# Kernel optimization log

Measured on AMD Instinct MI355X. Metric: run time of the kernel, lower is better.

## Reference

```python
import jax, jax.numpy as jnp
import numpy as np

M_MARGIN = 0.25
GAMMA = 256.0
NEG_INF = jnp.float32(-1e30)


def setup_inputs() -> dict:
    key = jax.random.key(0)
    k1, k2 = jax.random.split(key)
    feature = jax.random.normal(k1, (8192, 128), dtype=jnp.float32)
    label = jax.random.randint(k2, (8192,), 0, 64, dtype=jnp.int64)
    return {"feature": feature, "label": label}


def reference(feature, label):
    # F.normalize: L2-normalize rows (eps=1e-12)
    norm = jnp.maximum(jnp.linalg.norm(feature, axis=1, keepdims=True), 1e-12)
    f = feature / norm
    sim = f @ f.T  # [N, N]
    N = sim.shape[0]

    same = label[:, None] == label[None, :]
    triu = jnp.triu(jnp.ones((N, N), dtype=bool), k=1)
    pos_mask = same & triu
    neg_mask = (~same) & triu

    sim_d = jax.lax.stop_gradient(sim)  # .detach() in original
    ap = jnp.maximum(-sim_d + 1.0 + M_MARGIN, 0.0)
    an = jnp.maximum(sim_d + M_MARGIN, 0.0)
    delta_p = 1.0 - M_MARGIN
    delta_n = M_MARGIN

    logit_p = -ap * (sim - delta_p) * GAMMA
    logit_n = an * (sim - delta_n) * GAMMA

    # boolean-gather + logsumexp == masked logsumexp (fixed shapes, jit-friendly)
    lse_p = jax.nn.logsumexp(jnp.where(pos_mask, logit_p, NEG_INF))
    lse_n = jax.nn.logsumexp(jnp.where(neg_mask, logit_n, NEG_INF))

    return jax.nn.softplus(lse_n + lse_p)
```

## Files before the change

kernel.cpp:

```cpp
#include <hip/hip_runtime.h>
#include <hip/hip_bf16.h>
#include <math.h>

#define NROW 8192
#define DIM  128
#define BT   128
#define NT   (NROW / BT)
#define NBLK ((NT * (NT + 1)) / 2)
#define NWR  (NBLK * 4)

typedef __bf16 bf16x8 __attribute__((ext_vector_type(8)));
typedef float  f32x4  __attribute__((ext_vector_type(4)));

#define G2     369.3299304675746f
#define QPOS   (0.9375f * G2)
#define QNEG   (-0.0625f * G2)
#define NEGBIG (-3.0e38f)
#define MSENT  (-4000.0f)

__global__ __launch_bounds__(256)
void prep_kernel(const float* __restrict__ f, __hip_bfloat16* __restrict__ fhi) {
    int row  = blockIdx.x * 4 + (threadIdx.x >> 6);
    int lane = threadIdx.x & 63;
    float2 v = ((const float2*)(f + (size_t)row * DIM))[lane];
    float ss = v.x * v.x + v.y * v.y;
    #pragma unroll
    for (int off = 32; off; off >>= 1) ss += __shfl_xor(ss, off, 64);
    float inv = 1.0f / fmaxf(sqrtf(ss), 1e-12f);
    __hip_bfloat162 hv;
    hv.x = __float2bfloat16(v.x * inv);
    hv.y = __float2bfloat16(v.y * inv);
    ((__hip_bfloat162*)(fhi + (size_t)row * DIM))[lane] = hv;
}

__global__ __launch_bounds__(256, 2)
void sim_kernel(const __hip_bfloat16* __restrict__ fhi,
                const int* __restrict__ lab,
                float4* __restrict__ blockRes) {
    const int tid  = threadIdx.x;
    const int w    = tid >> 6;
    const int lane = tid & 63;
    const int lrow = lane & 15;
    const int lk   = lane >> 4;

    int bid = blockIdx.x;
    int tr = (int)((129.0f - sqrtf(16641.0f - 8.0f * (float)bid)) * 0.5f);
    while (tr > 0 && bid < tr * NT - (tr * (tr - 1)) / 2) --tr;
    while (bid >= (tr + 1) * NT - ((tr + 1) * tr) / 2) ++tr;
    const int tc = tr + (bid - (tr * NT - (tr * (tr - 1)) / 2));

    const int rowBase = tr * BT;
    const int colBase = tc * BT;
    const bool edge = (tr == tc);

    __shared__ __align__(16) char smem[64 * 1024];
    __shared__ int labA[BT];
    __shared__ int labB[BT];
    char* As = smem;
    char* Bs = smem + 32 * 1024;

    if (tid < BT)            labA[tid] = lab[rowBase + tid];
    else if (tid < 2 * BT)   labB[tid - BT] = lab[colBase + (tid - BT)];

    const int rsub4 = lane >> 4;
    const int col16 = (lane & 15) << 4;

    #pragma unroll
    for (int t = 0; t < 16; ++t) {
        int seg = w * 16 + t;
        int arr = seg >> 5;
        int s32 = seg & 31;
        int row = s32 * 4 + rsub4;
        const char* g = (const char*)fhi
            + (size_t)((arr ? colBase : rowBase) + row) * 256
            + (col16 ^ ((row & 7) << 4));
        char* ldsb = (arr ? Bs : As) + s32 * 1024;
        __builtin_amdgcn_global_load_lds(
            (const __attribute__((address_space(1))) void*)g,
            (__attribute__((address_space(3))) void*)ldsb, 16, 0, 0);
    }

    f32x4 acc[4][4];
    #pragma unroll
    for (int mi = 0; mi < 4; ++mi)
        #pragma unroll
        for (int ni = 0; ni < 4; ++ni) acc[mi][ni] = (f32x4){0.f, 0.f, 0.f, 0.f};

    const int mrow0 = (w >> 1) * 64;
    const int ncol0 = (w & 1) * 64;

    __syncthreads();

    #pragma unroll
    for (int q = 0; q < 4; ++q) {
        const int kb = q * 64 + lk * 16;
        bf16x8 bfr[4];
        #pragma unroll
        for (int ni = 0; ni < 4; ++ni) {
            int rb = colBase ? (ncol0 + ni * 16 + lrow) : (ncol0 + ni * 16 + lrow);
            rb = ncol0 + ni * 16 + lrow;
            bfr[ni] = *(const bf16x8*)(Bs + rb * 256 + (kb ^ ((rb & 7) << 4)));
        }
        bf16x8 afr[4];
        #pragma unroll
        for (int mi = 0; mi < 4; ++mi) {
            int ra = mrow0 + mi * 16 + lrow;
            afr[mi] = *(const bf16x8*)(As + ra * 256 + (kb ^ ((ra & 7) << 4)));
        }
        #pragma unroll
        for (int mi = 0; mi < 4; ++mi)
            #pragma unroll
            for (int ni = 0; ni < 4; ++ni)
                acc[mi][ni] = __builtin_amdgcn_mfma_f32_16x16x32_bf16(
                    afr[mi], bfr[ni], acc[mi][ni], 0, 0, 0);
    }

    int lbv[4];
    #pragma unroll
    for (int ni = 0; ni < 4; ++ni) lbv[ni] = labB[ncol0 + ni * 16 + lrow];
    int4 laR[4];
    #pragma unroll
    for (int mi = 0; mi < 4; ++mi)
        laR[mi] = *(const int4*)&labA[mrow0 + mi * 16 + lk * 4];

    float minp = 1e30f;
    float mabs = -1.0f;

#define PASS_A(EDGEF)                                                          \
    _Pragma("unroll")                                                          \
    for (int mi = 0; mi < 4; ++mi) {                                           \
        const int la[4] = {laR[mi].x, laR[mi].y, laR[mi].z, laR[mi].w};        \
        _Pragma("unroll")                                                      \
        for (int ni = 0; ni < 4; ++ni) {                                       \
            _Pragma("unroll")                                                  \
            for (int r = 0; r < 4; ++r) {                                      \
                float s = acc[mi][ni][r];                                      \
                bool pos = (la[r] == lbv[ni]);                                 \
                float t = fmaxf(s, -0.25f);                                    \
                bool valid = true;                                             \
                if (EDGEF) {                                                   \
                    int il = mrow0 + mi * 16 + lk * 4 + r;                     \
                    int jl = ncol0 + ni * 16 + lrow;                           \
                    valid = (jl > il);                                         \
                    pos = pos && valid;                                        \
                }                                                              \
                float u = pos ? s : t;                                         \
                minp = fminf(minp, pos ? s : 1e30f);                           \
                bool nm = EDGEF ? (valid && !pos) : !pos;                      \
                mabs = fmaxf(mabs, nm ? fabsf(t) : -1.0f);                     \
                acc[mi][ni][r] = u;                                            \
            }                                                                  \
        }                                                                      \
    }
    if (edge) { PASS_A(true) } else { PASS_A(false) }
#undef PASS_A

    #pragma unroll
    for (int off = 32; off; off >>= 1) {
        minp = fminf(minp, __shfl_xor(minp, off, 64));
        mabs = fmaxf(mabs, __shfl_xor(mabs, off, 64));
    }
    const float Mp = (minp < 2.0f)
        ? fmaf(G2, minp * minp, fmaf(-2.0f * G2, minp, QPOS)) : MSENT;
    const float Mn = (mabs >= 0.0f) ? fmaf(G2, mabs * mabs, QNEG) : MSENT;
    const float qph = QPOS - Mp;
    const float qnh = QNEG - Mn;
    float sp = 0.f, sn = 0.f;

#define PASS_B(EDGEF)                                                          \
    _Pragma("unroll")                                                          \
    for (int mi = 0; mi < 4; ++mi) {                                           \
        const int la[4] = {laR[mi].x, laR[mi].y, laR[mi].z, laR[mi].w};        \
        _Pragma("unroll")                                                      \
        for (int ni = 0; ni < 4; ++ni) {                                       \
            _Pragma("unroll")                                                  \
            for (int r = 0; r < 4; ++r) {                                      \
                float u = acc[mi][ni][r];                                      \
                bool pos = (la[r] == lbv[ni]);                                 \
                float P  = pos ? (-2.0f * G2) : 0.0f;                          \
                float Qh = pos ? qph : qnh;                                    \
                float e = __builtin_amdgcn_exp2f(                              \
                              fmaf(G2, u * u, fmaf(P, u, Qh)));                \
                if (EDGEF) {                                                   \
                    int il = mrow0 + mi * 16 + lk * 4 + r;                     \
                    int jl = ncol0 + ni * 16 + lrow;                           \
                    e = (jl > il) ? e : 0.f;                                   \
                }                                                              \
                float ep = pos ? e : 0.f;                                      \
                sp += ep;                                                      \
                sn += (e - ep);                                                \
            }                                                                  \
        }                                                                      \
    }
    if (edge) { PASS_B(true) } else { PASS_B(false) }
#undef PASS_B

    #pragma unroll
    for (int off = 32; off; off >>= 1) {
        sp += __shfl_xor(sp, off, 64);
        sn += __shfl_xor(sn, off, 64);
    }
    if (lane == 0) blockRes[bid * 4 + w] = make_float4(Mp, sp, Mn, sn);
}

__global__ __launch_bounds__(1024)
void final_kernel(const float4* __restrict__ waveRes, float* __restrict__ out) {
    __shared__ float red[16][4];
    const int tid  = threadIdx.x;
    const int wv   = tid >> 6;
    const int lane = tid & 63;

    float4 e[9];
    int ne = 0;
    for (int i = tid; i < NWR; i += 1024) e[ne++] = waveRes[i];

    float mp = NEGBIG, mn = NEGBIG;
    for (int k = 0; k < ne; ++k) {
        mp = fmaxf(mp, e[k].x);
        mn = fmaxf(mn, e[k].z);
    }
    #pragma unroll
    for (int off = 32; off; off >>= 1) {
        mp = fmaxf(mp, __shfl_xor(mp, off, 64));
        mn = fmaxf(mn, __shfl_xor(mn, off, 64));
    }
    if (lane == 0) { red[wv][0] = mp; red[wv][1] = mn; }
    __syncthreads();
    float MP = red[0][0], MN = red[0][1];
    #pragma unroll
    for (int q = 1; q < 16; ++q) {
        MP = fmaxf(MP, red[q][0]);
        MN = fmaxf(MN, red[q][1]);
    }

    float sp = 0.f, sn = 0.f;
    for (int k = 0; k < ne; ++k) {
        sp = fmaf(e[k].y, __builtin_amdgcn_exp2f(e[k].x - MP), sp);
        sn = fmaf(e[k].w, __builtin_amdgcn_exp2f(e[k].z - MN), sn);
    }
    #pragma unroll
    for (int off = 32; off; off >>= 1) {
        sp += __shfl_xor(sp, off, 64);
        sn += __shfl_xor(sn, off, 64);
    }
    __syncthreads();
    if (lane == 0) { red[wv][2] = sp; red[wv][3] = sn; }
    __syncthreads();
    if (tid == 0) {
        float Sp = 0.f, Sn = 0.f;
        #pragma unroll
        for (int q = 0; q < 16; ++q) { Sp += red[q][2]; Sn += red[q][3]; }
        const double LN2 = 0.6931471805599453;
        double lse_p = ((double)MP + log2((double)Sp)) * LN2;
        double lse_n = ((double)MN + log2((double)Sn)) * LN2;
        double xx = lse_p + lse_n;
        double r = (xx > 30.0) ? xx : log1p(exp(xx));
        out[0] = (float)r;
    }
}

extern "C" void kernel_launch(void* const* d_in, const int* in_sizes, int n_in,
                              void* d_out, int out_size, void* d_ws, size_t ws_size,
                              hipStream_t stream) {
    const float* f   = (const float*)d_in[0];
    const int*   lab = (const int*)d_in[1];
    float*  out      = (float*)d_out;

    __hip_bfloat16* fhi = (__hip_bfloat16*)d_ws;
    float4* blockRes = (float4*)((char*)d_ws + 4u * 1024 * 1024);

    prep_kernel<<<NROW / 4, 256, 0, stream>>>(f, fhi);
    sim_kernel<<<NBLK, 256, 0, stream>>>(fhi, lab, blockRes);
    final_kernel<<<1, 1024, 0, stream>>>(blockRes, out);
}
```

Baseline: 55.73 us.

## Sort rows by label so pure-negative tiles skip label masking

Adds a label histogram and prefix-sum kernel, then scatters the normalized rows into label-sorted order with an atomic cursor. Tiles whose row and column label ranges cannot overlap take a cheaper path with no positive branch and no per-element label comparisons. The sim kernel also moves to 512 threads with 8 waves on smaller 64x32 sub-tiles, and merges per-wave logsumexp partials into one result per block, which shrinks the final reduction. The cost is an extra launch plus atomics in prep, and the atomic scatter makes row order nondeterministic, which can change float summation order.

After: 51.67 us. -7.3%, faster.

```diff
diff --git a/kernel.cpp b/kernel.cpp
--- a/kernel.cpp
+++ b/kernel.cpp
@@ -7,7 +7,6 @@
 #define BT   128
 #define NT   (NROW / BT)
 #define NBLK ((NT * (NT + 1)) / 2)
-#define NWR  (NBLK * 4)
 
 typedef __bf16 bf16x8 __attribute__((ext_vector_type(8)));
 typedef float  f32x4  __attribute__((ext_vector_type(4)));
@@ -17,9 +16,35 @@
 #define QNEG   (-0.0625f * G2)
 #define NEGBIG (-3.0e38f)
 #define MSENT  (-4000.0f)
+#define CSTR   32
 
 __global__ __launch_bounds__(256)
-void prep_kernel(const float* __restrict__ f, __hip_bfloat16* __restrict__ fhi) {
+void hist_kernel(const int* __restrict__ lab, int* __restrict__ cursor) {
+    __shared__ int h[4][64];
+    const int tid  = threadIdx.x;
+    const int w    = tid >> 6;
+    const int lane = tid & 63;
+    h[w][lane] = 0;
+    __syncthreads();
+    for (int i = tid; i < NROW; i += 256)
+        atomicAdd(&h[w][lab[i]], 1);
+    __syncthreads();
+    if (tid < 64) {
+        int tot = h[0][tid] + h[1][tid] + h[2][tid] + h[3][tid];
+        int v = tot;
+        #pragma unroll
+        for (int off = 1; off < 64; off <<= 1) {
+            int u = __shfl_up(v, off, 64);
+            if (tid >= off) v += u;
+        }
+        cursor[tid * CSTR] = v - tot;
+    }
+}
+
+__global__ __launch_bounds__(256)
+void prep_kernel(const float* __restrict__ f, const int* __restrict__ lab,
+                 int* __restrict__ cursor,
+                 __hip_bfloat16* __restrict__ fhi, int* __restrict__ labS) {
     int row  = blockIdx.x * 4 + (threadIdx.x >> 6);
     int lane = threadIdx.x & 63;
     float2 v = ((const float2*)(f + (size_t)row * DIM))[lane];
@@ -27,15 +52,26 @@
     #pragma unroll
     for (int off = 32; off; off >>= 1) ss += __shfl_xor(ss, off, 64);
     float inv = 1.0f / fmaxf(sqrtf(ss), 1e-12f);
+    int l = lab[row];
+    int dest = 0;
+    if (lane == 0) dest = atomicAdd(&cursor[l * CSTR], 1);
+    dest = __shfl(dest, 0, 64);
     __hip_bfloat162 hv;
     hv.x = __float2bfloat16(v.x * inv);
     hv.y = __float2bfloat16(v.y * inv);
-    ((__hip_bfloat162*)(fhi + (size_t)row * DIM))[lane] = hv;
-}
-
-__global__ __launch_bounds__(256, 2)
+    ((__hip_bfloat162*)(fhi + (size_t)dest * DIM))[lane] = hv;
+    if (lane == 0) labS[dest] = l;
+}
+
+__device__ __forceinline__ void merge2(float& m, float& s, float mo, float so) {
+    float M = fmaxf(m, mo);
+    s = s * __builtin_amdgcn_exp2f(m - M) + so * __builtin_amdgcn_exp2f(mo - M);
+    m = M;
+}
+
+__global__ __launch_bounds__(512, 4)
 void sim_kernel(const __hip_bfloat16* __restrict__ fhi,
-                const int* __restrict__ lab,
+                const int* __restrict__ labS,
                 float4* __restrict__ blockRes) {
     const int tid  = threadIdx.x;
     const int w    = tid >> 6;
@@ -54,20 +90,16 @@
     const bool edge = (tr == tc);
 
     __shared__ __align__(16) char smem[64 * 1024];
-    __shared__ int labA[BT];
-    __shared__ int labB[BT];
+    __shared__ float red[8][4];
     char* As = smem;
     char* Bs = smem + 32 * 1024;
 
-    if (tid < BT)            labA[tid] = lab[rowBase + tid];
-    else if (tid < 2 * BT)   labB[tid - BT] = lab[colBase + (tid - BT)];
-
     const int rsub4 = lane >> 4;
     const int col16 = (lane & 15) << 4;
 
     #pragma unroll
-    for (int t = 0; t < 16; ++t) {
-        int seg = w * 16 + t;
+    for (int t = 0; t < 8; ++t) {
+        int seg = w * 8 + t;
         int arr = seg >> 5;
         int s32 = seg & 31;
         int row = s32 * 4 + rsub4;
@@ -80,58 +112,91 @@
             (__attribute__((address_space(3))) void*)ldsb, 16, 0, 0);
     }
 
-    f32x4 acc[4][4];
+    const bool pure = (!edge) && (labS[rowBase + BT - 1] != labS[colBase]);
+
+    const int mrow0 = (w >> 2) * 64;
+    const int ncol0 = (w & 3) * 32;
+
+    int lbv[2];
+    int4 laR[4];
+    if (!pure) {
+        #pragma unroll
+        for (int ni = 0; ni < 2; ++ni) lbv[ni] = labS[colBase + ncol0 + ni * 16 + lrow];
+        #pragma unroll
+        for (int mi = 0; mi < 4; ++mi)
+            laR[mi] = *(const int4*)&labS[rowBase + mrow0 + mi * 16 + lk * 4];
+    }
+
+    f32x4 acc[4][2];
     #pragma unroll
     for (int mi = 0; mi < 4; ++mi)
         #pragma unroll
-        for (int ni = 0; ni < 4; ++ni) acc[mi][ni] = (f32x4){0.f, 0.f, 0.f, 0.f};
-
-    const int mrow0 = (w >> 1) * 64;
-    const int ncol0 = (w & 1) * 64;
+        for (int ni = 0; ni < 2; ++ni) acc[mi][ni] = (f32x4){0.f, 0.f, 0.f, 0.f};
 
     __syncthreads();
 
     #pragma unroll
     for (int q = 0; q < 4; ++q) {
         const int kb = q * 64 + lk * 16;
-        bf16x8 bfr[4];
-        #pragma unroll
-        for (int ni = 0; ni < 4; ++ni) {
-            int rb = colBase ? (ncol0 + ni * 16 + lrow) : (ncol0 + ni * 16 + lrow);
-            rb = ncol0 + ni * 16 + lrow;
+        bf16x8 bfr[2];
+        #pragma unroll
+        for (int ni = 0; ni < 2; ++ni) {
+            int rb = ncol0 + ni * 16 + lrow;
             bfr[ni] = *(const bf16x8*)(Bs + rb * 256 + (kb ^ ((rb & 7) << 4)));
         }
-        bf16x8 afr[4];
         #pragma unroll
         for (int mi = 0; mi < 4; ++mi) {
             int ra = mrow0 + mi * 16 + lrow;
-            afr[mi] = *(const bf16x8*)(As + ra * 256 + (kb ^ ((ra & 7) << 4)));
-        }
+            bf16x8 afr = *(const bf16x8*)(As + ra * 256 + (kb ^ ((ra & 7) << 4)));
+            #pragma unroll
+            for (int ni = 0; ni < 2; ++ni)
+                acc[mi][ni] = __builtin_amdgcn_mfma_f32_16x16x32_bf16(
+                    afr, bfr[ni], acc[mi][ni], 0, 0, 0);
+        }
+    }
+
+    float Mp, Mn, sp, sn;
+    if (pure) {
+        float mx = 0.0f;
         #pragma unroll
         for (int mi = 0; mi < 4; ++mi)
             #pragma unroll
-            for (int ni = 0; ni < 4; ++ni)
-                acc[mi][ni] = __builtin_amdgcn_mfma_f32_16x16x32_bf16(
-                    afr[mi], bfr[ni], acc[mi][ni], 0, 0, 0);
-    }
-
-    int lbv[4];
-    #pragma unroll
-    for (int ni = 0; ni < 4; ++ni) lbv[ni] = labB[ncol0 + ni * 16 + lrow];
-    int4 laR[4];
-    #pragma unroll
-    for (int mi = 0; mi < 4; ++mi)
-        laR[mi] = *(const int4*)&labA[mrow0 + mi * 16 + lk * 4];
-
-    float minp = 1e30f;
-    float mabs = -1.0f;
+            for (int ni = 0; ni < 2; ++ni)
+                #pragma unroll
+                for (int r = 0; r < 4; ++r) {
+                    float t = fmaxf(acc[mi][ni][r], -0.25f);
+                    acc[mi][ni][r] = t;
+                    mx = fmaxf(mx, fabsf(t));
+                }
+        #pragma unroll
+        for (int off = 32; off; off >>= 1)
+            mx = fmaxf(mx, __shfl_xor(mx, off, 64));
+        const float zc = -G2 * mx * mx;
+        sn = 0.f;
+        #pragma unroll
+        for (int mi = 0; mi < 4; ++mi)
+            #pragma unroll
+            for (int ni = 0; ni < 2; ++ni)
+                #pragma unroll
+                for (int r = 0; r < 4; ++r) {
+                    float t = acc[mi][ni][r];
+                    sn += __builtin_amdgcn_exp2f(fmaf(G2, t * t, zc));
+                }
+        #pragma unroll
+        for (int off = 32; off; off >>= 1)
+            sn += __shfl_xor(sn, off, 64);
+        Mp = MSENT; sp = 0.f;
+        Mn = fmaf(G2, mx * mx, QNEG);
+    } else {
+        float minp = 1e30f;
+        float mabs = -1.0f;
 
 #define PASS_A(EDGEF)                                                          \
     _Pragma("unroll")                                                          \
     for (int mi = 0; mi < 4; ++mi) {                                           \
         const int la[4] = {laR[mi].x, laR[mi].y, laR[mi].z, laR[mi].w};        \
         _Pragma("unroll")                                                      \
-        for (int ni = 0; ni < 4; ++ni) {                                       \
+        for (int ni = 0; ni < 2; ++ni) {                                       \
             _Pragma("unroll")                                                  \
             for (int r = 0; r < 4; ++r) {                                      \
                 float s = acc[mi][ni][r];                                      \
@@ -152,27 +217,27 @@
             }                                                                  \
         }                                                                      \
     }
-    if (edge) { PASS_A(true) } else { PASS_A(false) }
+        if (edge) { PASS_A(true) } else { PASS_A(false) }
 #undef PASS_A
 
-    #pragma unroll
-    for (int off = 32; off; off >>= 1) {
-        minp = fminf(minp, __shfl_xor(minp, off, 64));
-        mabs = fmaxf(mabs, __shfl_xor(mabs, off, 64));
-    }
-    const float Mp = (minp < 2.0f)
-        ? fmaf(G2, minp * minp, fmaf(-2.0f * G2, minp, QPOS)) : MSENT;
-    const float Mn = (mabs >= 0.0f) ? fmaf(G2, mabs * mabs, QNEG) : MSENT;
-    const float qph = QPOS - Mp;
-    const float qnh = QNEG - Mn;
-    float sp = 0.f, sn = 0.f;
+        #pragma unroll
+        for (int off = 32; off; off >>= 1) {
+            minp = fminf(minp, __shfl_xor(minp, off, 64));
+            mabs = fmaxf(mabs, __shfl_xor(mabs, off, 64));
+        }
+        Mp = (minp < 2.0f)
+            ? fmaf(G2, minp * minp, fmaf(-2.0f * G2, minp, QPOS)) : MSENT;
+        Mn = (mabs >= 0.0f) ? fmaf(G2, mabs * mabs, QNEG) : MSENT;
+        const float qph = QPOS - Mp;
+        const float qnh = QNEG - Mn;
+        sp = 0.f; sn = 0.f;
 
 #define PASS_B(EDGEF)                                                          \
     _Pragma("unroll")                                                          \
     for (int mi = 0; mi < 4; ++mi) {                                           \
         const int la[4] = {laR[mi].x, laR[mi].y, laR[mi].z, laR[mi].w};        \
         _Pragma("unroll")                                                      \
-        for (int ni = 0; ni < 4; ++ni) {                                       \
+        for (int ni = 0; ni < 2; ++ni) {                                       \
             _Pragma("unroll")                                                  \
             for (int r = 0; r < 4; ++r) {                                      \
                 float u = acc[mi][ni][r];                                      \
@@ -192,27 +257,41 @@
             }                                                                  \
         }                                                                      \
     }
-    if (edge) { PASS_B(true) } else { PASS_B(false) }
+        if (edge) { PASS_B(true) } else { PASS_B(false) }
 #undef PASS_B
 
-    #pragma unroll
-    for (int off = 32; off; off >>= 1) {
-        sp += __shfl_xor(sp, off, 64);
-        sn += __shfl_xor(sn, off, 64);
-    }
-    if (lane == 0) blockRes[bid * 4 + w] = make_float4(Mp, sp, Mn, sn);
+        #pragma unroll
+        for (int off = 32; off; off >>= 1) {
+            sp += __shfl_xor(sp, off, 64);
+            sn += __shfl_xor(sn, off, 64);
+        }
+    }
+
+    if (lane == 0) {
+        red[w][0] = Mp; red[w][1] = sp; red[w][2] = Mn; red[w][3] = sn;
+    }
+    __syncthreads();
+    if (tid == 0) {
+        float mp = red[0][0], s_p = red[0][1], mn = red[0][2], s_n = red[0][3];
+        #pragma unroll
+        for (int q = 1; q < 8; ++q) {
+            merge2(mp, s_p, red[q][0], red[q][1]);
+            merge2(mn, s_n, red[q][2], red[q][3]);
+        }
+        blockRes[bid] = make_float4(mp, s_p, mn, s_n);
+    }
 }
 
 __global__ __launch_bounds__(1024)
-void final_kernel(const float4* __restrict__ waveRes, float* __restrict__ out) {
+void final_kernel(const float4* __restrict__ blockRes, float* __restrict__ out) {
     __shared__ float red[16][4];
     const int tid  = threadIdx.x;
     const int wv   = tid >> 6;
     const int lane = tid & 63;
 
-    float4 e[9];
+    float4 e[3];
     int ne = 0;
-    for (int i = tid; i < NWR; i += 1024) e[ne++] = waveRes[i];
+    for (int i = tid; i < NBLK; i += 1024) e[ne++] = blockRes[i];
 
     float mp = NEGBIG, mn = NEGBIG;
     for (int k = 0; k < ne; ++k) {
@@ -267,9 +346,12 @@
     float*  out      = (float*)d_out;
 
     __hip_bfloat16* fhi = (__hip_bfloat16*)d_ws;
+    int* labS    = (int*)((char*)d_ws + 2u * 1024 * 1024);
+    int* cursor  = (int*)((char*)d_ws + 3u * 1024 * 1024);
     float4* blockRes = (float4*)((char*)d_ws + 4u * 1024 * 1024);
 
-    prep_kernel<<<NROW / 4, 256, 0, stream>>>(f, fhi);
-    sim_kernel<<<NBLK, 256, 0, stream>>>(fhi, lab, blockRes);
+    hist_kernel<<<1, 256, 0, stream>>>(lab, cursor);
+    prep_kernel<<<NROW / 4, 256, 0, stream>>>(f, lab, cursor, fhi, labS);
+    sim_kernel<<<NBLK, 512, 0, stream>>>(fhi, labS, blockRes);
     final_kernel<<<1, 1024, 0, stream>>>(blockRes, out);
 }
```
